# Kernel optimization log

Hardware: AMD Instinct MI355X
Metric: run time of the kernel (lower is better)

The kernel has to match this reference:

```python
import jax, jax.numpy as jnp
import numpy as np

NT, NS, NH, NG, NR, NC = 365, 300, 128, 32, 8, 1


def _linear_params(key, fin, fout):
    k1, k2 = jax.random.split(key)
    s = 1.0 / np.sqrt(fin)
    W = jax.random.uniform(k1, (fout, fin), minval=-s, maxval=s, dtype=jnp.float32)
    b = jax.random.uniform(k2, (fout,), minval=-s, maxval=s, dtype=jnp.float32)
    return W, b


def setup_inputs() -> dict:
    key = jax.random.key(0)
    ks = jax.random.split(key, 9)
    x = jax.random.normal(ks[0], (NT, NS, 6), dtype=jnp.float32)
    xc = jax.random.normal(ks[1], (NS, NG), dtype=jnp.float32)
    fcR_w1, fcR_b1 = _linear_params(ks[2], NG, 256)
    fcR_w2, fcR_b2 = _linear_params(ks[3], 256, NH * NR)
    fcW_w1, fcW_b1 = _linear_params(ks[4], NG, 256)
    fcW_w2, fcW_b2 = _linear_params(ks[5], 256, NH * 7)
    fcT_w1, fcT_b1 = _linear_params(ks[6], 6 + NG, 256)
    fcT_w2, fcT_b2 = _linear_params(ks[7], 256, NH * 3)
    fcCT_w, fcCT_b = _linear_params(ks[8], 2 + NG, NC * NH * 3)
    return dict(x=x, xc=xc,
                fcR_w1=fcR_w1, fcR_b1=fcR_b1, fcR_w2=fcR_w2, fcR_b2=fcR_b2,
                fcW_w1=fcW_w1, fcW_b1=fcW_b1, fcW_w2=fcW_w2, fcW_b2=fcW_b2,
                fcT_w1=fcT_w1, fcT_b1=fcT_b1, fcT_w2=fcT_w2, fcT_b2=fcT_b2,
                fcCT_w=fcCT_w, fcCT_b=fcCT_b)


def _mlp(x, w1, b1, w2, b2):
    # Linear -> Tanh -> Dropout(identity in eval) -> Linear
    h = jnp.tanh(x @ w1.T + b1)
    return h @ w2.T + b2


def _conv_ts(q, r):
    # q: [nt, ns, nh]; r: [ns, nh, nr] routing weights. Causal temporal conv:
    # out[t] = sum_i q[t-i] * r[..., i]  (zero padded on the left)
    nt = q.shape[0]
    nr = r.shape[-1]
    qp = jnp.concatenate([jnp.zeros((nr - 1,) + q.shape[1:], q.dtype), q], axis=0)
    out = qp[nr - 1: nr - 1 + nt] * r[None, :, :, 0]
    for i in range(1, nr):
        out = out + qp[nr - 1 - i: nr - 1 - i + nt] * r[None, :, :, i]
    return out


def reference(x, xc, fcR_w1, fcR_b1, fcR_w2, fcR_b2,
              fcW_w1, fcW_b1, fcW_w2, fcW_b2,
              fcT_w1, fcT_b1, fcT_w2, fcT_b2,
              fcCT_w, fcCT_b):
    nh, nr = NH, NR
    P, E, T1, T2 = x[..., 0], x[..., 1], x[..., 2], x[..., 3]
    nt, ns = P.shape
    xcT = jnp.broadcast_to(xc[None], (nt, ns, xc.shape[-1]))
    xT = jnp.concatenate([x, xcT], axis=-1)                      # [nt, ns, 6+ng]

    # static gates per (site, bucket): sepPar with ['sigmoid']*4,'exp','relu','skip'
    w = _mlp(xc, fcW_w1, fcW_b1, fcW_w2, fcW_b2)                 # [ns, nh*7]
    kp = jax.nn.sigmoid(w[:, 0 * nh:1 * nh])
    ks_ = jax.nn.sigmoid(w[:, 1 * nh:2 * nh])
    kg = jax.nn.sigmoid(w[:, 2 * nh:3 * nh])
    gp = jax.nn.sigmoid(w[:, 3 * nh:4 * nh])
    gL = jnp.exp(w[:, 4 * nh:5 * nh]) * 2.0
    qb = jax.nn.relu(w[:, 5 * nh:6 * nh])
    ga = jax.nn.softmax(w[:, 6 * nh:7 * nh], axis=1)             # [ns, nh]

    # time-varying gates: ['skip','relu','exp']; vi overridden by hardsigmoid(v*2)
    v = _mlp(xT, fcT_w1, fcT_b1, fcT_w2, fcT_b2)                 # [nt, ns, nh*3]
    vi = jnp.clip(v[:, :, :nh] * 2.0 / 6.0 + 0.5, 0.0, 1.0)     # F.hardsigmoid(v*2)
    ve = jax.nn.relu(v[:, :, nh:2 * nh]) * 2.0
    vm = jnp.exp(v[:, :, 2 * nh:3 * nh])

    wR = _mlp(xc, fcR_w1, fcR_b1, fcR_w2, fcR_b2)                # [ns, nh*nr]
    r = jax.nn.relu(wR[:, :nh * nr]).reshape(ns, nh, nr)

    # snow fraction vf = arccos((T1+T2)/(T2-T1))/3.1415, overridden at extremes
    denom = T2 - T1
    ratio = jnp.clip((T1 + T2) / jnp.where(denom == 0, 1.0, denom), -1.0, 1.0)
    vf = jnp.arccos(ratio) / 3.1415
    vf = jnp.where(T1 >= 0, 0.0, jnp.where(T2 <= 0, 1.0, vf))
    Ps = P * vf                                                  # snow  [nt, ns]
    Pl = (P * (1.0 - vf))[:, :, None] * vi                       # rain  [nt, ns, nh]
    Ev = E[:, :, None] * ve                                      # evap  [nt, ns, nh]

    def step(carry, inp):
        Sf, Ss, Sg = carry
        Ps_k, Pl_k, Ev_k, vm_k = inp
        qf = jnp.minimum(Sf + Ps_k, vm_k)
        Sf = jax.nn.relu(Sf + Ps_k - vm_k)
        H = jax.nn.relu(Ss + Pl_k + qf - Ev_k)
        qp_ = jax.nn.relu(kp * (H - gL))
        qs = ks_ * jnp.minimum(H, gL)
        Ss = H - qp_ - qs
        qso = qs * (1.0 - gp)
        qsg = qs * gp
        qg = kg * (Sg + qsg) + qb
        Sg = (1.0 - kg) * (Sg + qsg) - qb
        return (Sf, Ss, Sg), (qp_, qso, qg)

    z = jnp.zeros((ns, nh), dtype=x.dtype)
    _, (Q1T, Q2T, Q3T) = jax.lax.scan(step, (z, z, z),
                                      (Ps[:, :, None], Pl, Ev, vm))

    Q1R = _conv_ts(Q1T, r)
    Q2R = _conv_ts(Q2T, r)
    Q3R = _conv_ts(Q3T, r)
    outQ = jnp.sum((Q1R + Q2R + Q3R) * ga, axis=2)               # [nt, ns]

    xTc = jnp.concatenate([T1[:, :, None], T2[:, :, None], xcT], axis=-1)
    wC = xTc @ fcCT_w.T + fcCT_b                                 # [nt, ns, nh*3]
    cp = jnp.exp(wC[:, :, 0 * nh:1 * nh])
    cs = jnp.exp(wC[:, :, 1 * nh:2 * nh])
    cg = jnp.exp(wC[:, :, 2 * nh:3 * nh])
    C1R = _conv_ts(Q1T * cp / 10.0, r)
    C2R = _conv_ts(Q2T * cs, r)
    C3R = _conv_ts(Q3T * cg, r)
    outC = jnp.sum((C1R + C2R + C3R) * ga, axis=2) / outQ
    return outQ, outC
```

## Files before the change

kernel.cpp:

```cpp
#include <hip/hip_runtime.h>
#include <math.h>

#define NTT 365
#define NSS 300
#define NROWS (NTT*NSS)
#define TPAD 384

using bf16x8 = __attribute__((ext_vector_type(8))) short;
using f32x4  = __attribute__((ext_vector_type(4))) float;

__device__ __forceinline__ float sigf(float v) { return 1.0f / (1.0f + __expf(-v)); }

__device__ __forceinline__ float tanhfast(float x) {
    float e = __expf(2.0f * x);
    return 1.0f - 2.0f * __builtin_amdgcn_rcpf(1.0f + e);
}

__device__ __forceinline__ unsigned short f2bf(float f) {
    unsigned u = __builtin_bit_cast(unsigned, f);
    u += 0x7FFFu + ((u >> 16) & 1u);
    return (unsigned short)(u >> 16);
}

__global__ __launch_bounds__(256) void k_prep(const float* __restrict__ w1,
                                              const float* __restrict__ w2,
                                              unsigned short* __restrict__ w1s,
                                              unsigned short* __restrict__ w2s)
{
    int G = blockIdx.x * 256 + threadIdx.x;
    if (G < 2048) {
        int lane = G & 63, ks = (G >> 6) & 1, tile = G >> 7;
        int o = tile * 16 + (lane & 15);
        int kb = ks * 32 + (lane >> 4) * 8;
        unsigned short tmp[8];
#pragma unroll
        for (int e = 0; e < 8; ++e) {
            int k = kb + e;
            tmp[e] = (k < 38) ? f2bf(w1[o * 38 + k]) : (unsigned short)0;
        }
        *(bf16x8*)(w1s + (size_t)G * 8) = *(bf16x8*)tmp;
    } else if (G < 2048 + 12288) {
        int G2 = G - 2048;
        int lane = G2 & 63, ks = (G2 >> 6) & 7, tile = G2 >> 9;
        int o = tile * 16 + (lane & 15);
        int kb = ks * 32 + (lane >> 4) * 8;
        unsigned short tmp[8];
#pragma unroll
        for (int e = 0; e < 8; ++e) tmp[e] = f2bf(w2[o * 256 + kb + e]);
        *(bf16x8*)(w2s + (size_t)G2 * 8) = *(bf16x8*)tmp;
    }
}

__global__ __launch_bounds__(256) void k_site(
    const float* __restrict__ xc,
    const float* __restrict__ wW1, const float* __restrict__ bW1,
    const float* __restrict__ wW2, const float* __restrict__ bW2,
    const float* __restrict__ wR1, const float* __restrict__ bR1,
    const float* __restrict__ wR2, const float* __restrict__ bR2,
    float* __restrict__ wsite, float* __restrict__ rsite)
{
    __shared__ float xcb[10][32];
    __shared__ float hW[10][256];
    __shared__ float hR[10][256];
    int tid = threadIdx.x;
    int s0 = blockIdx.x * 10;
    int os = blockIdx.y;
    for (int i = tid; i < 10 * 32; i += 256) xcb[i / 32][i % 32] = xc[s0 * 32 + i];
    __syncthreads();
    {
        int j = tid;
        float aW[10], aR[10];
#pragma unroll
        for (int r = 0; r < 10; ++r) { aW[r] = bW1[j]; aR[r] = bR1[j]; }
        for (int k = 0; k < 32; ++k) {
            float wv = wW1[j * 32 + k], rv = wR1[j * 32 + k];
#pragma unroll
            for (int r = 0; r < 10; ++r) { float xv = xcb[r][k]; aW[r] += xv * wv; aR[r] += xv * rv; }
        }
#pragma unroll
        for (int r = 0; r < 10; ++r) { hW[r][j] = tanhfast(aW[r]); hR[r][j] = tanhfast(aR[r]); }
    }
    __syncthreads();
    if (tid < 240) {
        int o_lin = os * 240 + tid;
        float acc[10];
        if (o_lin < 896) {
            int o = o_lin;
#pragma unroll
            for (int r = 0; r < 10; ++r) acc[r] = bW2[o];
            for (int k = 0; k < 256; ++k) {
                float wv = wW2[o * 256 + k];
#pragma unroll
                for (int r = 0; r < 10; ++r) acc[r] += hW[r][k] * wv;
            }
#pragma unroll
            for (int r = 0; r < 10; ++r) wsite[(s0 + r) * 896 + o] = acc[r];
        } else {
            int o = o_lin - 896;
#pragma unroll
            for (int r = 0; r < 10; ++r) acc[r] = bR2[o];
            for (int k = 0; k < 256; ++k) {
                float wv = wR2[o * 256 + k];
#pragma unroll
                for (int r = 0; r < 10; ++r) acc[r] += hR[r][k] * wv;
            }
#pragma unroll
            for (int r = 0; r < 10; ++r) rsite[(s0 + r) * 1024 + o] = acc[r];
        }
    }
}

__global__ __launch_bounds__(128) void k_softmax_ga(const float* __restrict__ wsite,
                                                    float* __restrict__ ga)
{
    int s = blockIdx.x, tid = threadIdx.x;
    __shared__ float red[2];
    float v = wsite[s * 896 + 6 * 128 + tid];
    float m = v;
#pragma unroll
    for (int off = 32; off >= 1; off >>= 1) m = fmaxf(m, __shfl_xor(m, off));
    if ((tid & 63) == 0) red[tid >> 6] = m;
    __syncthreads();
    m = fmaxf(red[0], red[1]);
    __syncthreads();
    float e = __expf(v - m);
    float ssum = e;
#pragma unroll
    for (int off = 32; off >= 1; off >>= 1) ssum += __shfl_xor(ssum, off);
    if ((tid & 63) == 0) red[tid >> 6] = ssum;
    __syncthreads();
    ssum = red[0] + red[1];
    ga[s * 128 + tid] = e / ssum;
}

__global__ __launch_bounds__(128) void k_ct(const float* __restrict__ xc,
                                            const float* __restrict__ ctw,
                                            const float* __restrict__ ctb,
                                            float* __restrict__ ctp8,
                                            float* __restrict__ ctpb)
{
    __shared__ float xcs[32];
    int s = blockIdx.x, h = threadIdx.x;
    if (h < 32) xcs[h] = xc[s * 32 + h];
    __syncthreads();
    const float L2E = 1.4426950408889634f;
    const float LG01 = -3.3219280948873623f;
    float out[8];
    float cgb = 0.0f;
#pragma unroll
    for (int g = 0; g < 3; ++g) {
        const float* wr = ctw + (g * 128 + h) * 34;
        float base = ctb[g * 128 + h];
        for (int k = 0; k < 32; ++k) base += wr[2 + k] * xcs[k];
        float w0 = wr[0] * L2E, w1 = wr[1] * L2E;
        float bb = base * L2E + ((g == 0) ? LG01 : 0.0f);
        if (g == 0) { out[0] = w0; out[1] = w1; out[2] = bb; }
        else if (g == 1) { out[3] = w0; out[4] = w1; out[5] = bb; }
        else { out[6] = w0; out[7] = w1; cgb = bb; }
    }
    float4* dst = (float4*)(ctp8 + ((size_t)s * 128 + h) * 8);
    dst[0] = make_float4(out[0], out[1], out[2], out[3]);
    dst[1] = make_float4(out[4], out[5], out[6], out[7]);
    ctpb[(size_t)s * 128 + h] = cgb;
}

__global__ __launch_bounds__(512) void k_fcT(
    const float* __restrict__ x, const float* __restrict__ xc,
    const unsigned short* __restrict__ w1s, const float* __restrict__ b1,
    const unsigned short* __restrict__ w2s, const float* __restrict__ b2,
    float4* __restrict__ PT, unsigned* __restrict__ NVu)
{
    __shared__ unsigned short A1[64][72];
    __shared__ unsigned short hb[64][264];
    __shared__ float2 pfE[64];
    int tid = threadIdx.x;
    int row0 = blockIdx.x * 64;

    for (int idx = tid; idx < 64 * 64; idx += 512) {
        int r = idx >> 6, c = idx & 63;
        int g = row0 + r;
        float val = 0.0f;
        if (g < NROWS) {
            if (c < 6) val = x[g * 6 + c];
            else if (c < 38) { int s = g % NSS; val = xc[s * 32 + (c - 6)]; }
        }
        A1[r][c] = f2bf(val);
    }
    if (tid < 64) {
        int r = tid, g = row0 + r;
        float P = 0, E = 0, T1 = 0, T2 = 0;
        if (g < NROWS) { P = x[g * 6]; E = x[g * 6 + 1]; T1 = x[g * 6 + 2]; T2 = x[g * 6 + 3]; }
        float den = T2 - T1;
        float dg = (den == 0.0f) ? 1.0f : den;
        float ratio = fminf(fmaxf((T1 + T2) / dg, -1.0f), 1.0f);
        float vf = acosf(ratio) * (1.0f / 3.1415f);
        vf = (T1 >= 0.0f) ? 0.0f : ((T2 <= 0.0f) ? 1.0f : vf);
        pfE[r] = make_float2(P * (1.0f - vf), 2.0f * E);
        if (g < NROWS) PT[g] = make_float4(P * vf, T1, T2, vf);
    }
    __syncthreads();

    int lane = tid & 63, wv = tid >> 6;
    int r16 = lane & 15;
    int kg = (lane >> 4) * 8;
    int rq = (lane >> 4) * 4;

    {
        int mt = wv & 3, nb = (wv >> 2) * 8;
        f32x4 acc[8];
#pragma unroll
        for (int i = 0; i < 8; ++i) acc[i] = (f32x4){0.f, 0.f, 0.f, 0.f};
#pragma unroll
        for (int ks = 0; ks < 2; ++ks) {
            bf16x8 a = *(const bf16x8*)&A1[mt * 16 + r16][ks * 32 + kg];
#pragma unroll
            for (int i = 0; i < 8; ++i) {
                bf16x8 b = *(const bf16x8*)(w1s + ((size_t)(((nb + i) * 2 + ks) * 64 + lane) << 3));
                acc[i] = __builtin_amdgcn_mfma_f32_16x16x32_bf16(a, b, acc[i], 0, 0, 0);
            }
        }
#pragma unroll
        for (int i = 0; i < 8; ++i) {
            int col = (nb + i) * 16 + r16;
            float bias = b1[col];
#pragma unroll
            for (int j = 0; j < 4; ++j) {
                int row = mt * 16 + rq + j;
                hb[row][col] = f2bf(tanhfast(acc[i][j] + bias));
            }
        }
    }
    __syncthreads();

    {
        int t0 = wv, t1 = wv + 8, t2 = wv + 16;
        f32x4 acc[4][3];
#pragma unroll
        for (int m = 0; m < 4; ++m)
#pragma unroll
            for (int c = 0; c < 3; ++c) acc[m][c] = (f32x4){0.f, 0.f, 0.f, 0.f};
#pragma unroll
        for (int ks = 0; ks < 8; ++ks) {
            bf16x8 b0 = *(const bf16x8*)(w2s + ((size_t)((t0 * 8 + ks) * 64 + lane) << 3));
            bf16x8 b1v = *(const bf16x8*)(w2s + ((size_t)((t1 * 8 + ks) * 64 + lane) << 3));
            bf16x8 b2v = *(const bf16x8*)(w2s + ((size_t)((t2 * 8 + ks) * 64 + lane) << 3));
#pragma unroll
            for (int m = 0; m < 4; ++m) {
                bf16x8 a = *(const bf16x8*)&hb[m * 16 + r16][ks * 32 + kg];
                acc[m][0] = __builtin_amdgcn_mfma_f32_16x16x32_bf16(a, b0, acc[m][0], 0, 0, 0);
                acc[m][1] = __builtin_amdgcn_mfma_f32_16x16x32_bf16(a, b1v, acc[m][1], 0, 0, 0);
                acc[m][2] = __builtin_amdgcn_mfma_f32_16x16x32_bf16(a, b2v, acc[m][2], 0, 0, 0);
            }
        }
        int hcol = wv * 16 + r16;
        float bias0 = b2[hcol], bias1 = b2[128 + hcol], bias2 = b2[256 + hcol];
#pragma unroll
        for (int m = 0; m < 4; ++m) {
            float2 pf[4];
#pragma unroll
            for (int j = 0; j < 4; ++j) pf[j] = pfE[m * 16 + rq + j];
#pragma unroll
            for (int j = 0; j < 4; ++j) {
                int r = m * 16 + rq + j;
                int g = row0 + r;
                if (g < NROWS) {
                    float vi = fminf(fmaxf((acc[m][0][j] + bias0) * (1.0f / 3.0f) + 0.5f, 0.0f), 1.0f);
                    float pl = pf[j].x * vi;
                    float ev = pf[j].y * fmaxf(acc[m][1][j] + bias1, 0.0f);
                    float vmv = __expf(acc[m][2][j] + bias2);
                    unsigned pk = (unsigned)f2bf(pl - ev) | ((unsigned)f2bf(vmv) << 16);
                    NVu[(size_t)g * 128 + hcol] = pk;
                }
            }
        }
    }
}

template<int ROLE>
__device__ __forceinline__ void scan_loop(
    int lane, int s, int half,
    float kp, float ks, float kg, float gp, float gpc, float gL, float kpgl, float qb,
    float r0, float r1, float r2, float r3, float r4, float r5, float r6, float r7,
    float cpw0, float cpw1, float cpb, float csw0, float csw1, float csb,
    float cgw0, float cgw1, float cgb,
    const unsigned* __restrict__ nvbase, const float4* ptlds, float (*red)[68],
    float* __restrict__ outp)
{
    float Sf = 0.0f, Ss = 0.0f, Sg = 0.0f;
    float a0 = 0, a1 = 0, a2 = 0, a3 = 0, a4 = 0, a5 = 0, a6 = 0, a7 = 0;
    unsigned nv[16];
#pragma unroll
    for (int i = 0; i < 16; ++i) nv[i] = nvbase[(size_t)i * NSS * 128];
    float4 pt[4];
#pragma unroll
    for (int i = 0; i < 4; ++i) pt[i] = ptlds[i];

    for (int tb = 0; tb < 368; tb += 16) {
#pragma unroll
        for (int u = 0; u < 16; ++u) {
            int t = tb + u;
            unsigned nvu = nv[u];
            float net = __builtin_bit_cast(float, nvu << 16);
            float vm  = __builtin_bit_cast(float, nvu & 0xFFFF0000u);
            nv[u] = nvbase[(size_t)(t + 16) * NSS * 128];
            float psv = pt[u & 3].x, T1 = pt[u & 3].y, T2 = pt[u & 3].z;
            pt[u & 3] = ptlds[t + 4];
            float t1v = Sf + psv;
            float qf = fminf(t1v, vm);
            Sf = fmaxf(t1v - vm, 0.0f);
            float H = fmaxf(Ss + qf + net, 0.0f);
            float qp = fmaxf(kp * H - kpgl, 0.0f);
            float qs = ks * fminf(H, gL);
            Ss = H - qp - qs;
            float qso = qs * gpc;
            float qsg = qs * gp;
            float tg = Sg + qsg;
            float qg = kg * tg + qb;
            Sg = tg - qg;
            float val;
            if (ROLE == 0) {
                val = qp + qso + qg;
            } else {
                float cp = exp2f(cpw0 * T1 + cpw1 * T2 + cpb);
                float cs = exp2f(csw0 * T1 + csw1 * T2 + csb);
                float cg = exp2f(cgw0 * T1 + cgw1 * T2 + cgb);
                val = qp * cp + qso * cs + qg * cg;
            }
            a0 += val * r0; a1 += val * r1; a2 += val * r2; a3 += val * r3;
            a4 += val * r4; a5 += val * r5; a6 += val * r6; a7 += val * r7;
            red[u & 7][lane] = a0;
            a0 = a1; a1 = a2; a2 = a3; a3 = a4; a4 = a5; a5 = a6; a6 = a7; a7 = 0.0f;
            if (u == 7 || u == 15) {
                int base = tb + ((u == 7) ? 0 : 8);
                int v = lane >> 3, sub = lane & 7;
                const float4* rp4 = (const float4*)&red[v][0];
                float4 b0 = rp4[sub * 2], b1 = rp4[sub * 2 + 1];
                float sm = ((b0.x + b0.y) + (b0.z + b0.w)) + ((b1.x + b1.y) + (b1.z + b1.w));
                sm += __shfl_xor(sm, 1);
                sm += __shfl_xor(sm, 2);
                sm += __shfl_xor(sm, 4);
                int tt = base + v;
                if (sub == 0 && tt < NTT) outp[((size_t)tt * NSS + s) * 2 + half] = sm;
            }
        }
    }
}

__global__ __launch_bounds__(64) void k_scan(
    const float* __restrict__ wsite, const float* __restrict__ rsite,
    const float* __restrict__ gaw,
    const float* __restrict__ ctp8, const float* __restrict__ ctpb,
    const float4* __restrict__ PTg, const unsigned* __restrict__ NVu,
    float* __restrict__ pQ, float* __restrict__ pC)
{
    __shared__ float4 ptlds[TPAD];
    __shared__ __align__(16) float red[8][68];
    int lane = threadIdx.x;
    int b = blockIdx.x;
    int role = b & 1;
    int half = (b >> 1) & 1;
    int s = b >> 2;
    int h = half * 64 + lane;

    for (int t = lane; t < TPAD; t += 64) ptlds[t] = PTg[(size_t)t * NSS + s];

    const float* wrow = wsite + s * 896;
    float kp = sigf(wrow[0 * 128 + h]);
    float ks = sigf(wrow[1 * 128 + h]);
    float kg = sigf(wrow[2 * 128 + h]);
    float gp = sigf(wrow[3 * 128 + h]);
    float gpc = 1.0f - gp;
    float gL = __expf(wrow[4 * 128 + h]) * 2.0f;
    float kpgl = kp * gL;
    float qb = fmaxf(wrow[5 * 128 + h], 0.0f);
    float ga = gaw[s * 128 + h];
    float r0 = fmaxf(rsite[s * 1024 + h * 8 + 0], 0.0f) * ga;
    float r1 = fmaxf(rsite[s * 1024 + h * 8 + 1], 0.0f) * ga;
    float r2 = fmaxf(rsite[s * 1024 + h * 8 + 2], 0.0f) * ga;
    float r3 = fmaxf(rsite[s * 1024 + h * 8 + 3], 0.0f) * ga;
    float r4 = fmaxf(rsite[s * 1024 + h * 8 + 4], 0.0f) * ga;
    float r5 = fmaxf(rsite[s * 1024 + h * 8 + 5], 0.0f) * ga;
    float r6 = fmaxf(rsite[s * 1024 + h * 8 + 6], 0.0f) * ga;
    float r7 = fmaxf(rsite[s * 1024 + h * 8 + 7], 0.0f) * ga;

    const unsigned* nvbase = NVu + (size_t)s * 128 + h;

    if (role == 0) {
        scan_loop<0>(lane, s, half, kp, ks, kg, gp, gpc, gL, kpgl, qb,
                     r0, r1, r2, r3, r4, r5, r6, r7,
                     0.f, 0.f, 0.f, 0.f, 0.f, 0.f, 0.f, 0.f, 0.f,
                     nvbase, ptlds, red, pQ);
    } else {
        const float4* cp4 = (const float4*)(ctp8 + ((size_t)s * 128 + h) * 8);
        float4 c0 = cp4[0], c1 = cp4[1];
        float cgb = ctpb[(size_t)s * 128 + h];
        scan_loop<1>(lane, s, half, kp, ks, kg, gp, gpc, gL, kpgl, qb,
                     r0, r1, r2, r3, r4, r5, r6, r7,
                     c0.x, c0.y, c0.z, c0.w, c1.x, c1.y, c1.z, c1.w, cgb,
                     nvbase, ptlds, red, pC);
    }
}

__global__ __launch_bounds__(256) void k_final(const float* __restrict__ pQ,
                                               const float* __restrict__ pC,
                                               float* __restrict__ out)
{
    int i = blockIdx.x * 256 + threadIdx.x;
    if (i < NROWS) {
        float q = pQ[i * 2] + pQ[i * 2 + 1];
        float c = pC[i * 2] + pC[i * 2 + 1];
        out[i] = q;
        out[NROWS + i] = c / q;
    }
}

extern "C" void kernel_launch(void* const* d_in, const int* in_sizes, int n_in,
                              void* d_out, int out_size, void* d_ws, size_t ws_size,
                              hipStream_t stream)
{
    const float* x      = (const float*)d_in[0];
    const float* xc     = (const float*)d_in[1];
    const float* fcR_w1 = (const float*)d_in[2];
    const float* fcR_b1 = (const float*)d_in[3];
    const float* fcR_w2 = (const float*)d_in[4];
    const float* fcR_b2 = (const float*)d_in[5];
    const float* fcW_w1 = (const float*)d_in[6];
    const float* fcW_b1 = (const float*)d_in[7];
    const float* fcW_w2 = (const float*)d_in[8];
    const float* fcW_b2 = (const float*)d_in[9];
    const float* fcT_w1 = (const float*)d_in[10];
    const float* fcT_b1 = (const float*)d_in[11];
    const float* fcT_w2 = (const float*)d_in[12];
    const float* fcT_b2 = (const float*)d_in[13];
    const float* fcCT_w = (const float*)d_in[14];
    const float* fcCT_b = (const float*)d_in[15];
    float* out = (float*)d_out;

    float* ws = (float*)d_ws;
    size_t o_w    = 0;
    size_t o_r    = o_w  + 300 * 896;
    size_t o_ga   = o_r  + 300 * 1024;
    size_t o_PT   = o_ga + 300 * 128;
    size_t o_NV   = o_PT + (size_t)TPAD * NSS * 4;
    size_t o_pQ   = o_NV + (size_t)TPAD * NSS * 128;
    size_t o_pC   = o_pQ + (size_t)NROWS * 2;
    size_t o_w1bf = o_pC + (size_t)NROWS * 2;
    size_t o_w2bf = o_w1bf + 8192;
    size_t o_ctp  = o_w2bf + 49152;
    size_t o_ctpb = o_ctp + (size_t)300 * 128 * 8;

    float* wsite = ws + o_w;
    float* rsite = ws + o_r;
    float* gaw   = ws + o_ga;
    float4* PT   = (float4*)(ws + o_PT);
    unsigned* NVu = (unsigned*)(ws + o_NV);
    float* pQ    = ws + o_pQ;
    float* pC    = ws + o_pC;
    unsigned short* w1s = (unsigned short*)(ws + o_w1bf);
    unsigned short* w2s = (unsigned short*)(ws + o_w2bf);
    float* ctp8  = ws + o_ctp;
    float* ctpb  = ws + o_ctpb;

    k_prep<<<56, 256, 0, stream>>>(fcT_w1, fcT_w2, w1s, w2s);
    k_site<<<dim3(30, 8), 256, 0, stream>>>(xc, fcW_w1, fcW_b1, fcW_w2, fcW_b2,
                                            fcR_w1, fcR_b1, fcR_w2, fcR_b2, wsite, rsite);
    k_softmax_ga<<<300, 128, 0, stream>>>(wsite, gaw);
    k_ct<<<300, 128, 0, stream>>>(xc, fcCT_w, fcCT_b, ctp8, ctpb);
    int nblk2 = (NROWS + 63) / 64;
    k_fcT<<<nblk2, 512, 0, stream>>>(x, xc, w1s, fcT_b1, w2s, fcT_b2, PT, NVu);
    k_scan<<<1200, 64, 0, stream>>>(wsite, rsite, gaw, ctp8, ctpb,
                                    PT, NVu, pQ, pC);
    k_final<<<(NROWS + 255) / 256, 256, 0, stream>>>(pQ, pC, out);
}
```

Baseline: 178.6 us.

## Split scan conv taps across two blocks, doubling grid and redundantly recomputing recurrence

```diff
diff --git a/kernel.cpp b/kernel.cpp
--- a/kernel.cpp
+++ b/kernel.cpp
@@ -276,24 +276,24 @@
     }
 }
 
-template<int ROLE>
+template<int TAPOFF, int ISC>
 __device__ __forceinline__ void scan_loop(
-    int lane, int s, int half,
+    int lane, int s, int outslot,
     float kp, float ks, float kg, float gp, float gpc, float gL, float kpgl, float qb,
-    float r0, float r1, float r2, float r3, float r4, float r5, float r6, float r7,
+    float r0, float r1, float r2, float r3,
     float cpw0, float cpw1, float cpb, float csw0, float csw1, float csb,
     float cgw0, float cgw1, float cgb,
-    const unsigned* __restrict__ nvbase, const float4* ptlds, float (*red)[68],
-    float* __restrict__ outp)
+    const unsigned* __restrict__ nvbase, const float4* __restrict__ PTg,
+    float (*red)[68], float* __restrict__ outp)
 {
     float Sf = 0.0f, Ss = 0.0f, Sg = 0.0f;
     float a0 = 0, a1 = 0, a2 = 0, a3 = 0, a4 = 0, a5 = 0, a6 = 0, a7 = 0;
     unsigned nv[16];
 #pragma unroll
     for (int i = 0; i < 16; ++i) nv[i] = nvbase[(size_t)i * NSS * 128];
-    float4 pt[4];
-#pragma unroll
-    for (int i = 0; i < 4; ++i) pt[i] = ptlds[i];
+    float4 pt[8];
+#pragma unroll
+    for (int i = 0; i < 8; ++i) pt[i] = PTg[(size_t)i * NSS + s];
 
     for (int tb = 0; tb < 368; tb += 16) {
 #pragma unroll
@@ -303,8 +303,8 @@
             float net = __builtin_bit_cast(float, nvu << 16);
             float vm  = __builtin_bit_cast(float, nvu & 0xFFFF0000u);
             nv[u] = nvbase[(size_t)(t + 16) * NSS * 128];
-            float psv = pt[u & 3].x, T1 = pt[u & 3].y, T2 = pt[u & 3].z;
-            pt[u & 3] = ptlds[t + 4];
+            float psv = pt[u & 7].x, T1 = pt[u & 7].y, T2 = pt[u & 7].z;
+            pt[u & 7] = PTg[(size_t)(t + 8) * NSS + s];
             float t1v = Sf + psv;
             float qf = fminf(t1v, vm);
             Sf = fmaxf(t1v - vm, 0.0f);
@@ -318,29 +318,38 @@
             float qg = kg * tg + qb;
             Sg = tg - qg;
             float val;
-            if (ROLE == 0) {
-                val = qp + qso + qg;
-            } else {
+            if (ISC) {
                 float cp = exp2f(cpw0 * T1 + cpw1 * T2 + cpb);
                 float cs = exp2f(csw0 * T1 + csw1 * T2 + csb);
                 float cg = exp2f(cgw0 * T1 + cgw1 * T2 + cgb);
                 val = qp * cp + qso * cs + qg * cg;
-            }
-            a0 += val * r0; a1 += val * r1; a2 += val * r2; a3 += val * r3;
-            a4 += val * r4; a5 += val * r5; a6 += val * r6; a7 += val * r7;
-            red[u & 7][lane] = a0;
+            } else {
+                val = qp + qso + qg;
+            }
+            if (TAPOFF == 0) {
+                a0 += val * r0; a1 += val * r1; a2 += val * r2; a3 += val * r3;
+            } else {
+                a4 += val * r0; a5 += val * r1; a6 += val * r2; a7 += val * r3;
+            }
+            red[u][lane] = a0;
             a0 = a1; a1 = a2; a2 = a3; a3 = a4; a4 = a5; a5 = a6; a6 = a7; a7 = 0.0f;
-            if (u == 7 || u == 15) {
-                int base = tb + ((u == 7) ? 0 : 8);
-                int v = lane >> 3, sub = lane & 7;
+            if (u == 15) {
+                int v = lane >> 2, sub = lane & 3;
                 const float4* rp4 = (const float4*)&red[v][0];
-                float4 b0 = rp4[sub * 2], b1 = rp4[sub * 2 + 1];
-                float sm = ((b0.x + b0.y) + (b0.z + b0.w)) + ((b1.x + b1.y) + (b1.z + b1.w));
+                float4 x0 = rp4[sub * 4 + 0];
+                float4 x1 = rp4[sub * 4 + 1];
+                float4 x2 = rp4[sub * 4 + 2];
+                float4 x3 = rp4[sub * 4 + 3];
+                float sA = (x0.x + x0.y) + (x0.z + x0.w);
+                float sB = (x1.x + x1.y) + (x1.z + x1.w);
+                float sC = (x2.x + x2.y) + (x2.z + x2.w);
+                float sD = (x3.x + x3.y) + (x3.z + x3.w);
+                float sm = (sA + sB) + (sC + sD);
                 sm += __shfl_xor(sm, 1);
                 sm += __shfl_xor(sm, 2);
-                sm += __shfl_xor(sm, 4);
-                int tt = base + v;
-                if (sub == 0 && tt < NTT) outp[((size_t)tt * NSS + s) * 2 + half] = sm;
+                int tt = tb + v;
+                if (sub == 0 && tt < NTT)
+                    outp[((size_t)tt * NSS + s) * 4 + outslot] = sm;
             }
         }
     }
@@ -353,16 +362,15 @@
     const float4* __restrict__ PTg, const unsigned* __restrict__ NVu,
     float* __restrict__ pQ, float* __restrict__ pC)
 {
-    __shared__ float4 ptlds[TPAD];
-    __shared__ __align__(16) float red[8][68];
+    __shared__ __align__(16) float red[16][68];
     int lane = threadIdx.x;
     int b = blockIdx.x;
-    int role = b & 1;
+    int tg  = b & 1;
     int half = (b >> 1) & 1;
-    int s = b >> 2;
+    int isc = (b >> 2) & 1;
+    int s = b >> 3;
     int h = half * 64 + lane;
-
-    for (int t = lane; t < TPAD; t += 64) ptlds[t] = PTg[(size_t)t * NSS + s];
+    int outslot = half * 2 + tg;
 
     const float* wrow = wsite + s * 896;
     float kp = sigf(wrow[0 * 128 + h]);
@@ -374,30 +382,37 @@
     float kpgl = kp * gL;
     float qb = fmaxf(wrow[5 * 128 + h], 0.0f);
     float ga = gaw[s * 128 + h];
-    float r0 = fmaxf(rsite[s * 1024 + h * 8 + 0], 0.0f) * ga;
-    float r1 = fmaxf(rsite[s * 1024 + h * 8 + 1], 0.0f) * ga;
-    float r2 = fmaxf(rsite[s * 1024 + h * 8 + 2], 0.0f) * ga;
-    float r3 = fmaxf(rsite[s * 1024 + h * 8 + 3], 0.0f) * ga;
-    float r4 = fmaxf(rsite[s * 1024 + h * 8 + 4], 0.0f) * ga;
-    float r5 = fmaxf(rsite[s * 1024 + h * 8 + 5], 0.0f) * ga;
-    float r6 = fmaxf(rsite[s * 1024 + h * 8 + 6], 0.0f) * ga;
-    float r7 = fmaxf(rsite[s * 1024 + h * 8 + 7], 0.0f) * ga;
+    float4 rr = *(const float4*)(rsite + s * 1024 + h * 8 + tg * 4);
+    float r0 = fmaxf(rr.x, 0.0f) * ga;
+    float r1 = fmaxf(rr.y, 0.0f) * ga;
+    float r2 = fmaxf(rr.z, 0.0f) * ga;
+    float r3 = fmaxf(rr.w, 0.0f) * ga;
 
     const unsigned* nvbase = NVu + (size_t)s * 128 + h;
 
-    if (role == 0) {
-        scan_loop<0>(lane, s, half, kp, ks, kg, gp, gpc, gL, kpgl, qb,
-                     r0, r1, r2, r3, r4, r5, r6, r7,
-                     0.f, 0.f, 0.f, 0.f, 0.f, 0.f, 0.f, 0.f, 0.f,
-                     nvbase, ptlds, red, pQ);
+    if (isc == 0) {
+        if (tg == 0)
+            scan_loop<0, 0>(lane, s, outslot, kp, ks, kg, gp, gpc, gL, kpgl, qb,
+                            r0, r1, r2, r3, 0.f, 0.f, 0.f, 0.f, 0.f, 0.f, 0.f, 0.f, 0.f,
+                            nvbase, PTg, red, pQ);
+        else
+            scan_loop<4, 0>(lane, s, outslot, kp, ks, kg, gp, gpc, gL, kpgl, qb,
+                            r0, r1, r2, r3, 0.f, 0.f, 0.f, 0.f, 0.f, 0.f, 0.f, 0.f, 0.f,
+                            nvbase, PTg, red, pQ);
     } else {
         const float4* cp4 = (const float4*)(ctp8 + ((size_t)s * 128 + h) * 8);
         float4 c0 = cp4[0], c1 = cp4[1];
         float cgb = ctpb[(size_t)s * 128 + h];
-        scan_loop<1>(lane, s, half, kp, ks, kg, gp, gpc, gL, kpgl, qb,
-                     r0, r1, r2, r3, r4, r5, r6, r7,
-                     c0.x, c0.y, c0.z, c0.w, c1.x, c1.y, c1.z, c1.w, cgb,
-                     nvbase, ptlds, red, pC);
+        if (tg == 0)
+            scan_loop<0, 1>(lane, s, outslot, kp, ks, kg, gp, gpc, gL, kpgl, qb,
+                            r0, r1, r2, r3,
+                            c0.x, c0.y, c0.z, c0.w, c1.x, c1.y, c1.z, c1.w, cgb,
+                            nvbase, PTg, red, pC);
+        else
+            scan_loop<4, 1>(lane, s, outslot, kp, ks, kg, gp, gpc, gL, kpgl, qb,
+                            r0, r1, r2, r3,
+                            c0.x, c0.y, c0.z, c0.w, c1.x, c1.y, c1.z, c1.w, cgb,
+                            nvbase, PTg, red, pC);
     }
 }
 
@@ -407,8 +422,10 @@
 {
     int i = blockIdx.x * 256 + threadIdx.x;
     if (i < NROWS) {
-        float q = pQ[i * 2] + pQ[i * 2 + 1];
-        float c = pC[i * 2] + pC[i * 2 + 1];
+        float4 q4 = *(const float4*)(pQ + (size_t)i * 4);
+        float4 c4 = *(const float4*)(pC + (size_t)i * 4);
+        float q = (q4.x + q4.y) + (q4.z + q4.w);
+        float c = (c4.x + c4.y) + (c4.z + c4.w);
         out[i] = q;
         out[NROWS + i] = c / q;
     }
@@ -443,8 +460,8 @@
     size_t o_PT   = o_ga + 300 * 128;
     size_t o_NV   = o_PT + (size_t)TPAD * NSS * 4;
     size_t o_pQ   = o_NV + (size_t)TPAD * NSS * 128;
-    size_t o_pC   = o_pQ + (size_t)NROWS * 2;
-    size_t o_w1bf = o_pC + (size_t)NROWS * 2;
+    size_t o_pC   = o_pQ + (size_t)NROWS * 4;
+    size_t o_w1bf = o_pC + (size_t)NROWS * 4;
     size_t o_w2bf = o_w1bf + 8192;
     size_t o_ctp  = o_w2bf + 49152;
     size_t o_ctpb = o_ctp + (size_t)300 * 128 * 8;
@@ -468,7 +485,7 @@
     k_ct<<<300, 128, 0, stream>>>(xc, fcCT_w, fcCT_b, ctp8, ctpb);
     int nblk2 = (NROWS + 63) / 64;
     k_fcT<<<nblk2, 512, 0, stream>>>(x, xc, w1s, fcT_b1, w2s, fcT_b2, PT, NVu);
-    k_scan<<<1200, 64, 0, stream>>>(wsite, rsite, gaw, ctp8, ctpb,
+    k_scan<<<2400, 64, 0, stream>>>(wsite, rsite, gaw, ctp8, ctpb,
                                     PT, NVu, pQ, pC);
     k_final<<<(NROWS + 255) / 256, 256, 0, stream>>>(pQ, pC, out);
 }
```

New measurement: 212.8 us. 19.2% more time.

## Store NV/PT site-major and restructure scan with double-buffered prefetch and 16-step reductions

Applied to the files above, without the earlier changes.

```diff
diff --git a/kernel.cpp b/kernel.cpp
--- a/kernel.cpp
+++ b/kernel.cpp
@@ -4,7 +4,7 @@
 #define NTT 365
 #define NSS 300
 #define NROWS (NTT*NSS)
-#define TPAD 384
+#define TPAD2 416
 
 using bf16x8 = __attribute__((ext_vector_type(8))) short;
 using f32x4  = __attribute__((ext_vector_type(4))) float;
@@ -168,7 +168,7 @@
     const float* __restrict__ x, const float* __restrict__ xc,
     const unsigned short* __restrict__ w1s, const float* __restrict__ b1,
     const unsigned short* __restrict__ w2s, const float* __restrict__ b2,
-    float4* __restrict__ PT, unsigned* __restrict__ NVu)
+    float4* __restrict__ PTt, unsigned* __restrict__ NVu)
 {
     __shared__ unsigned short A1[64][72];
     __shared__ unsigned short hb[64][264];
@@ -196,7 +196,10 @@
         float vf = acosf(ratio) * (1.0f / 3.1415f);
         vf = (T1 >= 0.0f) ? 0.0f : ((T2 <= 0.0f) ? 1.0f : vf);
         pfE[r] = make_float2(P * (1.0f - vf), 2.0f * E);
-        if (g < NROWS) PT[g] = make_float4(P * vf, T1, T2, vf);
+        if (g < NROWS) {
+            int tg = g / NSS, sg = g - tg * NSS;
+            PTt[(size_t)sg * TPAD2 + tg] = make_float4(P * vf, T1, T2, vf);
+        }
     }
     __syncthreads();
 
@@ -269,80 +272,93 @@
                     float ev = pf[j].y * fmaxf(acc[m][1][j] + bias1, 0.0f);
                     float vmv = __expf(acc[m][2][j] + bias2);
                     unsigned pk = (unsigned)f2bf(pl - ev) | ((unsigned)f2bf(vmv) << 16);
-                    NVu[(size_t)g * 128 + hcol] = pk;
+                    int tg = g / NSS, sg = g - tg * NSS;
+                    NVu[((size_t)sg * TPAD2 + tg) * 128 + hcol] = pk;
                 }
             }
         }
     }
 }
 
-template<int ROLE>
+template<int ISC>
 __device__ __forceinline__ void scan_loop(
     int lane, int s, int half,
     float kp, float ks, float kg, float gp, float gpc, float gL, float kpgl, float qb,
     float r0, float r1, float r2, float r3, float r4, float r5, float r6, float r7,
     float cpw0, float cpw1, float cpb, float csw0, float csw1, float csb,
     float cgw0, float cgw1, float cgb,
-    const unsigned* __restrict__ nvbase, const float4* ptlds, float (*red)[68],
+    const unsigned* __restrict__ nvsite, const float4* ptlds, float (*red)[68],
     float* __restrict__ outp)
 {
     float Sf = 0.0f, Ss = 0.0f, Sg = 0.0f;
     float a0 = 0, a1 = 0, a2 = 0, a3 = 0, a4 = 0, a5 = 0, a6 = 0, a7 = 0;
-    unsigned nv[16];
-#pragma unroll
-    for (int i = 0; i < 16; ++i) nv[i] = nvbase[(size_t)i * NSS * 128];
+    unsigned A[16], B[16];
     float4 pt[4];
 #pragma unroll
+    for (int i = 0; i < 16; ++i) A[i] = nvsite[(size_t)i * 128];
+#pragma unroll
     for (int i = 0; i < 4; ++i) pt[i] = ptlds[i];
 
-    for (int tb = 0; tb < 368; tb += 16) {
-#pragma unroll
-        for (int u = 0; u < 16; ++u) {
-            int t = tb + u;
-            unsigned nvu = nv[u];
-            float net = __builtin_bit_cast(float, nvu << 16);
-            float vm  = __builtin_bit_cast(float, nvu & 0xFFFF0000u);
-            nv[u] = nvbase[(size_t)(t + 16) * NSS * 128];
-            float psv = pt[u & 3].x, T1 = pt[u & 3].y, T2 = pt[u & 3].z;
-            pt[u & 3] = ptlds[t + 4];
-            float t1v = Sf + psv;
-            float qf = fminf(t1v, vm);
-            Sf = fmaxf(t1v - vm, 0.0f);
-            float H = fmaxf(Ss + qf + net, 0.0f);
-            float qp = fmaxf(kp * H - kpgl, 0.0f);
-            float qs = ks * fminf(H, gL);
-            Ss = H - qp - qs;
-            float qso = qs * gpc;
-            float qsg = qs * gp;
-            float tg = Sg + qsg;
-            float qg = kg * tg + qb;
-            Sg = tg - qg;
-            float val;
-            if (ROLE == 0) {
-                val = qp + qso + qg;
-            } else {
-                float cp = exp2f(cpw0 * T1 + cpw1 * T2 + cpb);
-                float cs = exp2f(csw0 * T1 + csw1 * T2 + csb);
-                float cg = exp2f(cgw0 * T1 + cgw1 * T2 + cgb);
-                val = qp * cp + qso * cs + qg * cg;
-            }
-            a0 += val * r0; a1 += val * r1; a2 += val * r2; a3 += val * r3;
-            a4 += val * r4; a5 += val * r5; a6 += val * r6; a7 += val * r7;
-            red[u & 7][lane] = a0;
-            a0 = a1; a1 = a2; a2 = a3; a3 = a4; a4 = a5; a5 = a6; a6 = a7; a7 = 0.0f;
-            if (u == 7 || u == 15) {
-                int base = tb + ((u == 7) ? 0 : 8);
-                int v = lane >> 3, sub = lane & 7;
-                const float4* rp4 = (const float4*)&red[v][0];
-                float4 b0 = rp4[sub * 2], b1 = rp4[sub * 2 + 1];
-                float sm = ((b0.x + b0.y) + (b0.z + b0.w)) + ((b1.x + b1.y) + (b1.z + b1.w));
-                sm += __shfl_xor(sm, 1);
-                sm += __shfl_xor(sm, 2);
-                sm += __shfl_xor(sm, 4);
-                int tt = base + v;
-                if (sub == 0 && tt < NTT) outp[((size_t)tt * NSS + s) * 2 + half] = sm;
-            }
-        }
+    auto STEP = [&](int t, int uu, unsigned nvu, unsigned& pref) {
+        pref = nvsite[(size_t)(t + 16) * 128];
+        float net = __builtin_bit_cast(float, nvu << 16);
+        float vm  = __builtin_bit_cast(float, nvu & 0xFFFF0000u);
+        int ps = uu & 3;
+        float psv = pt[ps].x, T1 = pt[ps].y, T2 = pt[ps].z;
+        pt[ps] = ptlds[t + 4];
+        float t1v = Sf + psv;
+        float qf = fminf(t1v, vm);
+        Sf = fmaxf(t1v - vm, 0.0f);
+        float H = fmaxf(Ss + qf + net, 0.0f);
+        float qp = fmaxf(kp * H - kpgl, 0.0f);
+        float qs = ks * fminf(H, gL);
+        Ss = H - qp - qs;
+        float qso = qs * gpc;
+        float qsg = qs * gp;
+        float tg2 = Sg + qsg;
+        float qg = kg * tg2 + qb;
+        Sg = tg2 - qg;
+        float val;
+        if (ISC) {
+            float cp = exp2f(cpw0 * T1 + cpw1 * T2 + cpb);
+            float cs = exp2f(csw0 * T1 + csw1 * T2 + csb);
+            float cg = exp2f(cgw0 * T1 + cgw1 * T2 + cgb);
+            val = qp * cp + qso * cs + qg * cg;
+        } else {
+            val = qp + qso + qg;
+        }
+        a0 += val * r0; a1 += val * r1; a2 += val * r2; a3 += val * r3;
+        a4 += val * r4; a5 += val * r5; a6 += val * r6; a7 += val * r7;
+        red[uu & 15][lane] = a0;
+        a0 = a1; a1 = a2; a2 = a3; a3 = a4; a4 = a5; a5 = a6; a6 = a7; a7 = 0.0f;
+    };
+
+    auto RED = [&](int base) {
+        int v = lane >> 2, sub = lane & 3;
+        const float4* rp4 = (const float4*)&red[v][0];
+        float4 x0 = rp4[sub * 4 + 0];
+        float4 x1 = rp4[sub * 4 + 1];
+        float4 x2 = rp4[sub * 4 + 2];
+        float4 x3 = rp4[sub * 4 + 3];
+        float sA = (x0.x + x0.y) + (x0.z + x0.w);
+        float sB = (x1.x + x1.y) + (x1.z + x1.w);
+        float sC = (x2.x + x2.y) + (x2.z + x2.w);
+        float sD = (x3.x + x3.y) + (x3.z + x3.w);
+        float sm = (sA + sB) + (sC + sD);
+        sm += __shfl_xor(sm, 1);
+        sm += __shfl_xor(sm, 2);
+        int tt = base + v;
+        if (sub == 0 && tt < NTT)
+            outp[((size_t)tt * NSS + s) * 2 + half] = sm;
+    };
+
+    for (int tb = 0; tb < 384; tb += 32) {
+#pragma unroll
+        for (int u = 0; u < 16; ++u) STEP(tb + u, u, A[u], B[u]);
+        RED(tb);
+#pragma unroll
+        for (int u = 0; u < 16; ++u) STEP(tb + 16 + u, u + 16, B[u], A[u]);
+        RED(tb + 16);
     }
 }
 
@@ -350,19 +366,20 @@
     const float* __restrict__ wsite, const float* __restrict__ rsite,
     const float* __restrict__ gaw,
     const float* __restrict__ ctp8, const float* __restrict__ ctpb,
-    const float4* __restrict__ PTg, const unsigned* __restrict__ NVu,
+    const float4* __restrict__ PTt, const unsigned* __restrict__ NVu,
     float* __restrict__ pQ, float* __restrict__ pC)
 {
-    __shared__ float4 ptlds[TPAD];
-    __shared__ __align__(16) float red[8][68];
+    __shared__ float4 ptlds[TPAD2];
+    __shared__ __align__(16) float red[16][68];
     int lane = threadIdx.x;
     int b = blockIdx.x;
-    int role = b & 1;
-    int half = (b >> 1) & 1;
-    int s = b >> 2;
+    int s = (b >> 5) * 8 + (b & 7);
+    int hr = (b >> 3) & 3;
+    int half = hr >> 1, role = hr & 1;
+    if (s >= NSS) return;
     int h = half * 64 + lane;
 
-    for (int t = lane; t < TPAD; t += 64) ptlds[t] = PTg[(size_t)t * NSS + s];
+    for (int t = lane; t < TPAD2; t += 64) ptlds[t] = PTt[(size_t)s * TPAD2 + t];
 
     const float* wrow = wsite + s * 896;
     float kp = sigf(wrow[0 * 128 + h]);
@@ -374,22 +391,24 @@
     float kpgl = kp * gL;
     float qb = fmaxf(wrow[5 * 128 + h], 0.0f);
     float ga = gaw[s * 128 + h];
-    float r0 = fmaxf(rsite[s * 1024 + h * 8 + 0], 0.0f) * ga;
-    float r1 = fmaxf(rsite[s * 1024 + h * 8 + 1], 0.0f) * ga;
-    float r2 = fmaxf(rsite[s * 1024 + h * 8 + 2], 0.0f) * ga;
-    float r3 = fmaxf(rsite[s * 1024 + h * 8 + 3], 0.0f) * ga;
-    float r4 = fmaxf(rsite[s * 1024 + h * 8 + 4], 0.0f) * ga;
-    float r5 = fmaxf(rsite[s * 1024 + h * 8 + 5], 0.0f) * ga;
-    float r6 = fmaxf(rsite[s * 1024 + h * 8 + 6], 0.0f) * ga;
-    float r7 = fmaxf(rsite[s * 1024 + h * 8 + 7], 0.0f) * ga;
-
-    const unsigned* nvbase = NVu + (size_t)s * 128 + h;
+    float4 rrA = *(const float4*)(rsite + s * 1024 + h * 8);
+    float4 rrB = *(const float4*)(rsite + s * 1024 + h * 8 + 4);
+    float r0 = fmaxf(rrA.x, 0.0f) * ga;
+    float r1 = fmaxf(rrA.y, 0.0f) * ga;
+    float r2 = fmaxf(rrA.z, 0.0f) * ga;
+    float r3 = fmaxf(rrA.w, 0.0f) * ga;
+    float r4 = fmaxf(rrB.x, 0.0f) * ga;
+    float r5 = fmaxf(rrB.y, 0.0f) * ga;
+    float r6 = fmaxf(rrB.z, 0.0f) * ga;
+    float r7 = fmaxf(rrB.w, 0.0f) * ga;
+
+    const unsigned* nvsite = NVu + (size_t)s * TPAD2 * 128 + h;
 
     if (role == 0) {
         scan_loop<0>(lane, s, half, kp, ks, kg, gp, gpc, gL, kpgl, qb,
                      r0, r1, r2, r3, r4, r5, r6, r7,
                      0.f, 0.f, 0.f, 0.f, 0.f, 0.f, 0.f, 0.f, 0.f,
-                     nvbase, ptlds, red, pQ);
+                     nvsite, ptlds, red, pQ);
     } else {
         const float4* cp4 = (const float4*)(ctp8 + ((size_t)s * 128 + h) * 8);
         float4 c0 = cp4[0], c1 = cp4[1];
@@ -397,7 +416,7 @@
         scan_loop<1>(lane, s, half, kp, ks, kg, gp, gpc, gL, kpgl, qb,
                      r0, r1, r2, r3, r4, r5, r6, r7,
                      c0.x, c0.y, c0.z, c0.w, c1.x, c1.y, c1.z, c1.w, cgb,
-                     nvbase, ptlds, red, pC);
+                     nvsite, ptlds, red, pC);
     }
 }
 
@@ -441,8 +460,8 @@
     size_t o_r    = o_w  + 300 * 896;
     size_t o_ga   = o_r  + 300 * 1024;
     size_t o_PT   = o_ga + 300 * 128;
-    size_t o_NV   = o_PT + (size_t)TPAD * NSS * 4;
-    size_t o_pQ   = o_NV + (size_t)TPAD * NSS * 128;
+    size_t o_NV   = o_PT + (size_t)TPAD2 * NSS * 4;
+    size_t o_pQ   = o_NV + (size_t)TPAD2 * NSS * 128;
     size_t o_pC   = o_pQ + (size_t)NROWS * 2;
     size_t o_w1bf = o_pC + (size_t)NROWS * 2;
     size_t o_w2bf = o_w1bf + 8192;
@@ -452,7 +471,7 @@
     float* wsite = ws + o_w;
     float* rsite = ws + o_r;
     float* gaw   = ws + o_ga;
-    float4* PT   = (float4*)(ws + o_PT);
+    float4* PTt  = (float4*)(ws + o_PT);
     unsigned* NVu = (unsigned*)(ws + o_NV);
     float* pQ    = ws + o_pQ;
     float* pC    = ws + o_pC;
@@ -467,8 +486,8 @@
     k_softmax_ga<<<300, 128, 0, stream>>>(wsite, gaw);
     k_ct<<<300, 128, 0, stream>>>(xc, fcCT_w, fcCT_b, ctp8, ctpb);
     int nblk2 = (NROWS + 63) / 64;
-    k_fcT<<<nblk2, 512, 0, stream>>>(x, xc, w1s, fcT_b1, w2s, fcT_b2, PT, NVu);
-    k_scan<<<1200, 64, 0, stream>>>(wsite, rsite, gaw, ctp8, ctpb,
-                                    PT, NVu, pQ, pC);
+    k_fcT<<<nblk2, 512, 0, stream>>>(x, xc, w1s, fcT_b1, w2s, fcT_b2, PTt, NVu);
+    k_scan<<<1216, 64, 0, stream>>>(wsite, rsite, gaw, ctp8, ctpb,
+                                    PTt, NVu, pQ, pC);
     k_final<<<(NROWS + 255) / 256, 256, 0, stream>>>(pQ, pC, out);
 }
```

After: 175.6 us. Within noise of the previous version (-1.7%).
